# Optimization experiments

Hardware: AMD Instinct MI355X
Metric: run time of the kernel (lower is better)

## Reference

```python
import jax, jax.numpy as jnp
import numpy as np

N, IN_DIM, HID, E, NUM_TASKS, TED = 8192, 1024, 2048, 4, 8, 100
MU = 0.01
EPS = 1e-6


def setup_inputs() -> dict:
    key = jax.random.key(0)
    ks = jax.random.split(key, 8)
    s_in = 1.0 / np.sqrt(IN_DIM)
    s_h = 1.0 / np.sqrt(HID)
    return {
        "backbone_output": jax.random.normal(ks[0], (N, IN_DIM), dtype=jnp.float32),
        "task": jax.random.randint(ks[1], (N,), 0, NUM_TASKS),
        "task_embeddings": jax.random.normal(ks[2], (NUM_TASKS, TED), dtype=jnp.float32),
        "routing_matrix": jax.random.normal(ks[3], (IN_DIM + TED, E), dtype=jnp.float32) * 0.05,
        "W1": jax.random.uniform(ks[4], (E, IN_DIM, HID), jnp.float32, -s_in, s_in),
        "b1": jax.random.uniform(ks[5], (E, HID), jnp.float32, -s_in, s_in),
        "W2": jax.random.uniform(ks[6], (E, HID, HID), jnp.float32, -s_h, s_h),
        "b2": jax.random.uniform(ks[7], (E, HID), jnp.float32, -s_h, s_h),
    }


def _gram_schmidt(x):
    # x: [N, E, H] -> orthonormal basis along expert axis via sequential GS
    b0 = x[:, 0] / jnp.linalg.norm(x[:, 0], axis=-1, keepdims=True)
    basis = [b0]
    for i in range(1, x.shape[1]):
        v = x[:, i]                           # [N, H]
        B = jnp.stack(basis, axis=1)          # [N, i, H]
        coef = jnp.einsum("nh,nih->ni", v, B)
        w = v - jnp.einsum("ni,nih->nh", coef, B)
        basis.append(w / jnp.linalg.norm(w, axis=-1, keepdims=True))
    return jnp.stack(basis, axis=1)           # [N, E, H]


def reference(backbone_output, task, task_embeddings, routing_matrix, W1, b1, W2, b2):
    # router: softmax over experts on [x ; task_emb[task]] @ R
    router_in = jnp.concatenate([backbone_output, task_embeddings[task]], axis=-1)
    weights = jax.nn.softmax(router_in @ routing_matrix, axis=-1)   # [N, E]

    # per-expert 2-layer ReLU MLP, all experts at once
    h = jax.nn.relu(jnp.einsum("ni,eih->neh", backbone_output, W1) + b1[None])
    expert_outputs = jax.nn.relu(jnp.einsum("neh,ehk->nek", h, W2) + b2[None])  # [N,E,H]

    # top-1 gate: keep only max weight, zero the rest
    idx = jnp.argmax(weights, axis=-1)
    gates = jnp.where(jnp.arange(weights.shape[-1])[None, :] == idx[:, None], weights, 0.0)

    ortho = _gram_schmidt(expert_outputs)
    tower_input = jnp.einsum("ne,neh->nh", gates, ortho)

    reg_loss = -(1.0 / E) * MU * jnp.sum(jnp.log(gates + EPS), axis=-1)
    return tower_input, reg_loss
```

## Files before the change

kernel.cpp:

```cpp
#include <hip/hip_runtime.h>
#include <hip/hip_bf16.h>
#include <cstdint>

#define N_SAMP 8192
#define IN_DIM 1024
#define HID    2048
#define NE     4

typedef __attribute__((ext_vector_type(8))) __bf16 bf16x8;
typedef __attribute__((ext_vector_type(4))) float  f32x4;

#define MFMA16 __builtin_amdgcn_mfma_f32_16x16x32_bf16

__device__ __forceinline__ unsigned short f2b(float f) {
    unsigned u = __float_as_uint(f);
    u += 0x7fff + ((u >> 16) & 1);
    return (unsigned short)(u >> 16);
}
__device__ __forceinline__ float b2f(unsigned short s) {
    return __uint_as_float(((unsigned)s) << 16);
}

__device__ __forceinline__ void gll16(const void* g, void* l) {
    __builtin_amdgcn_global_load_lds(
        (const __attribute__((address_space(1))) void*)g,
        (__attribute__((address_space(3))) void*)l,
        16, 0, 0);
}

__device__ __forceinline__ int swz(int byte) {
    return byte ^ (((byte >> 7) & 7) << 4);
}

__global__ void transpose_conv(const float* __restrict__ src, unsigned short* __restrict__ dst,
                               int K, int M, size_t srcStride, size_t dstStride) {
    __shared__ float tile[64][65];
    const int e  = blockIdx.z;
    const int k0 = blockIdx.x * 64, m0 = blockIdx.y * 64;
    const int t  = threadIdx.x;
    const int tc = t & 15, tr = t >> 4;
    const float* s = src + (size_t)e * srcStride + (size_t)k0 * M + m0;
    #pragma unroll
    for (int r = tr; r < 64; r += 16) {
        float4 v = *(const float4*)&s[(size_t)r * M + tc * 4];
        tile[r][tc * 4 + 0] = v.x; tile[r][tc * 4 + 1] = v.y;
        tile[r][tc * 4 + 2] = v.z; tile[r][tc * 4 + 3] = v.w;
    }
    __syncthreads();
    unsigned short* d = dst + (size_t)e * dstStride + (size_t)m0 * K + k0;
    #pragma unroll
    for (int r = tr; r < 64; r += 16) {
        ushort4 o;
        o.x = f2b(tile[tc * 4 + 0][r]); o.y = f2b(tile[tc * 4 + 1][r]);
        o.z = f2b(tile[tc * 4 + 2][r]); o.w = f2b(tile[tc * 4 + 3][r]);
        *(ushort4*)&d[(size_t)r * K + tc * 4] = o;
    }
}

__global__ __launch_bounds__(256) void router_kernel(
    const float* __restrict__ bb, const int* __restrict__ task,
    const float* __restrict__ temb, const float* __restrict__ rm,
    unsigned short* __restrict__ Abf,
    float* __restrict__ gval, int* __restrict__ gidx,
    float* __restrict__ regout) {
    const int t = threadIdx.x, wave = t >> 6, lane = t & 63;
    const int n = blockIdx.x * 4 + wave;
    const int tk = task[n];
    float a0 = 0.f, a1 = 0.f, a2 = 0.f, a3 = 0.f;
    for (int i = lane; i < IN_DIM + 100; i += 64) {
        float x;
        if (i < IN_DIM) {
            x = bb[(size_t)n * IN_DIM + i];
            Abf[(size_t)n * IN_DIM + i] = f2b(x);
        } else {
            x = temb[tk * 100 + (i - IN_DIM)];
        }
        float4 r = *(const float4*)&rm[i * 4];
        a0 += x * r.x; a1 += x * r.y; a2 += x * r.z; a3 += x * r.w;
    }
    #pragma unroll
    for (int o = 32; o; o >>= 1) {
        a0 += __shfl_xor(a0, o); a1 += __shfl_xor(a1, o);
        a2 += __shfl_xor(a2, o); a3 += __shfl_xor(a3, o);
    }
    if (lane == 0) {
        float l[4] = {a0, a1, a2, a3};
        float mx = fmaxf(fmaxf(l[0], l[1]), fmaxf(l[2], l[3]));
        float ex[4], s = 0.f;
        #pragma unroll
        for (int j = 0; j < 4; j++) { ex[j] = expf(l[j] - mx); s += ex[j]; }
        int bi = 0; float bw = ex[0];
        #pragma unroll
        for (int j = 1; j < 4; j++) if (ex[j] > bw) { bw = ex[j]; bi = j; }
        float g = bw / s;
        gval[n] = g;
        gidx[n] = bi;
        regout[n] = -0.0025f * (logf(g + 1e-6f) + 3.0f * logf(1e-6f));
    }
}

__global__ void compact_kernel(const int* __restrict__ gidx, int* __restrict__ list,
                               int* __restrict__ pos, int* __restrict__ cnt) {
    const int e = blockIdx.x;
    const int t = threadIdx.x, lane = t & 63, wave = t >> 6;
    __shared__ int wbase[4];
    __shared__ int running;
    if (t == 0) running = 0;
    __syncthreads();
    int* le = list + (size_t)e * N_SAMP;
    int* pe = pos + (size_t)e * N_SAMP;
    for (int base = 0; base < N_SAMP; base += 256) {
        const int n = base + t;
        const bool f = gidx[n] >= e;
        unsigned long long m = __ballot(f);
        int rank = __popcll(m & ((1ULL << lane) - 1ULL));
        if (lane == 0) wbase[wave] = __popcll(m);
        __syncthreads();
        int wb = 0;
        #pragma unroll
        for (int w = 0; w < 4; w++) if (w < wave) wb += wbase[w];
        int tot = wbase[0] + wbase[1] + wbase[2] + wbase[3];
        int o = running + wb + rank;
        if (f) { le[o] = n; pe[n] = o; }
        __syncthreads();
        if (t == 0) running += tot;
        __syncthreads();
    }
    const int c = running;
    if (t == 0) cnt[e] = c;
    const int padded = (c + 255) & ~255;
    for (int i = c + t; i < padded && i < N_SAMP; i += 256) le[i] = 0;
}

template<int KT>
__device__ __forceinline__ void gemm_core(
    const unsigned short* __restrict__ A, const unsigned short* __restrict__ BT,
    const float* __restrict__ bias, unsigned short* __restrict__ C,
    int M, const int* __restrict__ rowlist, const int* __restrict__ cntp,
    int bid, char* lds_) {
    constexpr int nt = KT / 64;
    const int cnt = *cntp;
    const int mb = bid & 7, nb = bid >> 3;
    const int n0 = nb * 256;
    if (n0 >= cnt) return;
    const int m0 = mb * 256;
    const int t = threadIdx.x;
    const int w = t >> 6, lane = t & 63;
    const int wm = w >> 2, wn = w & 3;
    const int lrow = lane & 15, kg = lane >> 4;

    int rr[2], cb[2];
    #pragma unroll
    for (int q = 0; q < 2; q++) {
        int Ps = swz((t + q * 512) * 16);
        rr[q] = Ps >> 7;
        cb[q] = Ps & 127;
    }
    const char* aS[2][2];
    const char* bS[2][2];
    #pragma unroll
    for (int h = 0; h < 2; h++)
        #pragma unroll
        for (int q = 0; q < 2; q++) {
            int r = n0 + h * 128 + rr[q];
            int ga = rowlist ? rowlist[r] : r;
            aS[h][q] = (const char*)A + (size_t)ga * (KT * 2) + cb[q];
            bS[h][q] = (const char*)BT + (size_t)(m0 + h * 128 + rr[q]) * (KT * 2) + cb[q];
        }

    auto stageA = [&](int buf, int h, int kt) {
        gll16(aS[h][0] + kt * 128, lds_ + buf * 65536 + h * 16384 + w * 1024);
        gll16(aS[h][1] + kt * 128, lds_ + buf * 65536 + h * 16384 + 8192 + w * 1024);
    };
    auto stageB = [&](int buf, int h, int kt) {
        gll16(bS[h][0] + kt * 128, lds_ + buf * 65536 + 32768 + h * 16384 + w * 1024);
        gll16(bS[h][1] + kt * 128, lds_ + buf * 65536 + 32768 + h * 16384 + 8192 + w * 1024);
    };

    const int mask = (lrow & 7) << 4;
    const int c0 = (kg * 16) ^ mask;
    const int c1 = (kg * 16 + 64) ^ mask;
    const char* const pA[2] = { lds_ + wm * 16384 + lrow * 128 + c0,
                                lds_ + wm * 16384 + lrow * 128 + c1 };
    const int browB = (wn & 1) * 64 + lrow;
    const char* const pB[2] = { lds_ + 32768 + (wn >> 1) * 16384 + browB * 128 + c0,
                                lds_ + 32768 + (wn >> 1) * 16384 + browB * 128 + c1 };
    auto ldA = [&](int buf, int i, int kk) -> bf16x8 {
        return *(const bf16x8*)(pA[kk] + buf * 65536 + i * 2048);
    };
    auto ldB = [&](int buf, int j, int kk) -> bf16x8 {
        return *(const bf16x8*)(pB[kk] + buf * 65536 + j * 2048);
    };

    f32x4 acc[8][4];
    #pragma unroll
    for (int i = 0; i < 8; i++)
        #pragma unroll
        for (int j = 0; j < 4; j++) acc[i][j] = (f32x4){0.f, 0.f, 0.f, 0.f};

    stageA(0, 0, 0); stageA(0, 1, 0); stageB(0, 0, 0); stageB(0, 1, 0);
    stageA(1, 0, 1); stageA(1, 1, 1); stageB(1, 0, 1);
    asm volatile("s_waitcnt vmcnt(6)" ::: "memory");
    __builtin_amdgcn_s_barrier();

    bf16x8 af[4][2], bfr[4][2];
    auto tile = [&](int kt, int buf) {
        #pragma unroll
        for (int i = 0; i < 4; i++) { af[i][0] = ldA(buf, i, 0); af[i][1] = ldA(buf, i, 1); }
        #pragma unroll
        for (int j = 0; j < 2; j++) { bfr[j][0] = ldB(buf, j, 0); bfr[j][1] = ldB(buf, j, 1); }
        if (kt + 1 < nt) stageB(buf ^ 1, 1, kt + 1);
        __builtin_amdgcn_s_barrier();
        __builtin_amdgcn_s_setprio(1);
        #pragma unroll
        for (int i = 0; i < 4; i++)
            #pragma unroll
            for (int j = 0; j < 2; j++) {
                acc[i][j] = MFMA16(af[i][0], bfr[j][0], acc[i][j], 0, 0, 0);
                acc[i][j] = MFMA16(af[i][1], bfr[j][1], acc[i][j], 0, 0, 0);
            }
        __builtin_amdgcn_s_setprio(0);
        __builtin_amdgcn_s_barrier();
        #pragma unroll
        for (int j = 2; j < 4; j++) { bfr[j][0] = ldB(buf, j, 0); bfr[j][1] = ldB(buf, j, 1); }
        __builtin_amdgcn_s_barrier();
        __builtin_amdgcn_s_setprio(1);
        #pragma unroll
        for (int i = 0; i < 4; i++)
            #pragma unroll
            for (int j = 0; j < 2; j++) {
                acc[i][2 + j] = MFMA16(af[i][0], bfr[2 + j][0], acc[i][2 + j], 0, 0, 0);
                acc[i][2 + j] = MFMA16(af[i][1], bfr[2 + j][1], acc[i][2 + j], 0, 0, 0);
            }
        __builtin_amdgcn_s_setprio(0);
        __builtin_amdgcn_s_barrier();
        #pragma unroll
        for (int i = 0; i < 4; i++) { af[i][0] = ldA(buf, 4 + i, 0); af[i][1] = ldA(buf, 4 + i, 1); }
        if (kt + 2 < nt) stageB(buf, 0, kt + 2);
        __builtin_amdgcn_s_barrier();
        __builtin_amdgcn_s_setprio(1);
        #pragma unroll
        for (int i = 0; i < 4; i++)
            #pragma unroll
            for (int j = 0; j < 2; j++) {
                acc[4 + i][j] = MFMA16(af[i][0], bfr[j][0], acc[4 + i][j], 0, 0, 0);
                acc[4 + i][j] = MFMA16(af[i][1], bfr[j][1], acc[4 + i][j], 0, 0, 0);
            }
        __builtin_amdgcn_s_setprio(0);
        __builtin_amdgcn_s_barrier();
        if (kt + 2 < nt) { stageA(buf, 0, kt + 2); stageA(buf, 1, kt + 2); }
        __builtin_amdgcn_s_barrier();
        __builtin_amdgcn_s_setprio(1);
        #pragma unroll
        for (int i = 0; i < 4; i++)
            #pragma unroll
            for (int j = 0; j < 2; j++) {
                acc[4 + i][2 + j] = MFMA16(af[i][0], bfr[2 + j][0], acc[4 + i][2 + j], 0, 0, 0);
                acc[4 + i][2 + j] = MFMA16(af[i][1], bfr[2 + j][1], acc[4 + i][2 + j], 0, 0, 0);
            }
        __builtin_amdgcn_s_setprio(0);
        if (kt < nt - 2) asm volatile("s_waitcnt vmcnt(6)" ::: "memory");
        else             asm volatile("s_waitcnt vmcnt(0)" ::: "memory");
        __builtin_amdgcn_s_barrier();
    };
    for (int kt = 0; kt < nt; kt += 2) { tile(kt, 0); tile(kt + 1, 1); }

    float bv[4];
    #pragma unroll
    for (int j = 0; j < 4; j++)
        bv[j] = bias[m0 + wn * 64 + j * 16 + lrow];
    #pragma unroll
    for (int i = 0; i < 8; i++) {
        const int srow0 = n0 + wm * 128 + i * 16 + kg * 4;
        #pragma unroll
        for (int j = 0; j < 4; j++) {
            const int col = m0 + wn * 64 + j * 16 + lrow;
            #pragma unroll
            for (int q = 0; q < 4; q++) {
                if (srow0 + q < cnt) {
                    float x = acc[i][j][q] + bv[j];
                    C[(size_t)(srow0 + q) * M + col] = f2b(fmaxf(x, 0.f));
                }
            }
        }
    }
}

template<int KT>
__global__ __launch_bounds__(512, 2) void gemm256(
    const unsigned short* __restrict__ A, const unsigned short* __restrict__ BT,
    const float* __restrict__ bias, unsigned short* __restrict__ C,
    int M, const int* __restrict__ rowlist, const int* __restrict__ cntp) {
    extern __shared__ char lds_[];
    gemm_core<KT>(A, BT, bias, C, M, rowlist, cntp, blockIdx.x, lds_);
}

__global__ __launch_bounds__(512, 2) void gemm256_dual(
    const unsigned short* __restrict__ A2, const unsigned short* __restrict__ BT2,
    const float* __restrict__ bias2, unsigned short* __restrict__ C2,
    const int* __restrict__ cnt2,
    const unsigned short* __restrict__ A1, const unsigned short* __restrict__ BT1,
    const float* __restrict__ bias1, unsigned short* __restrict__ C1,
    const int* __restrict__ rowlist1, const int* __restrict__ cnt1) {
    extern __shared__ char lds_[];
    const int bid = blockIdx.x;
    if (bid < 256) {
        gemm_core<HID>(A2, BT2, bias2, C2, HID, nullptr, cnt2, bid, lds_);
    } else {
        gemm_core<IN_DIM>(A1, BT1, bias1, C1, HID, rowlist1, cnt1, bid - 256, lds_);
    }
}

__global__ __launch_bounds__(512, 2) void gemm256_dual_g1g1(
    const unsigned short* __restrict__ A,
    const unsigned short* __restrict__ BTa, const float* __restrict__ biasa,
    unsigned short* __restrict__ Ca, const int* __restrict__ rla, const int* __restrict__ cnta,
    const unsigned short* __restrict__ BTb, const float* __restrict__ biasb,
    unsigned short* __restrict__ Cb, const int* __restrict__ rlb, const int* __restrict__ cntb) {
    extern __shared__ char lds_[];
    const int bid = blockIdx.x;
    if (bid < 256) {
        gemm_core<IN_DIM>(A, BTa, biasa, Ca, HID, rla, cnta, bid, lds_);
    } else {
        gemm_core<IN_DIM>(A, BTb, biasb, Cb, HID, rlb, cntb, bid - 256, lds_);
    }
}

__global__ __launch_bounds__(512, 2) void gemm256_dual_g2g2(
    const unsigned short* __restrict__ Aa, const unsigned short* __restrict__ BTa,
    const float* __restrict__ biasa, unsigned short* __restrict__ Ca, const int* __restrict__ cnta,
    const unsigned short* __restrict__ Ab, const unsigned short* __restrict__ BTb,
    const float* __restrict__ biasb, unsigned short* __restrict__ Cb, const int* __restrict__ cntb) {
    extern __shared__ char lds_[];
    const int bid = blockIdx.x;
    if (bid < 256) {
        gemm_core<HID>(Aa, BTa, biasa, Ca, HID, nullptr, cnta, bid, lds_);
    } else {
        gemm_core<HID>(Ab, BTb, biasb, Cb, HID, nullptr, cntb, bid - 256, lds_);
    }
}

__global__ __launch_bounds__(256, 1) void gs_kernel(
    const unsigned short* __restrict__ eo, const float* __restrict__ gval,
    const int* __restrict__ gidx, const int* __restrict__ pos,
    float* __restrict__ dout) {
    const int t = threadIdx.x, wave = t >> 6, lane = t & 63;
    const int n = blockIdx.x * 4 + wave;
    const int idx = gidx[n];
    const float g = gval[n];

    float v[32], b0[32], b1[32], b2[32];

    auto loadv = [&](float* dst, int e) {
        const size_t row = pos[(size_t)e * N_SAMP + n];
        const unsigned short* p = eo + ((size_t)e * N_SAMP + row) * HID + lane * 8;
        #pragma unroll
        for (int c = 0; c < 4; c++) {
            uint4 u = *(const uint4*)(p + c * 512);
            const unsigned short* us = (const unsigned short*)&u;
            #pragma unroll
            for (int j = 0; j < 8; j++) dst[c * 8 + j] = b2f(us[j]);
        }
    };
    auto wdot = [&](const float* x, const float* y) -> float {
        float s = 0.f;
        #pragma unroll
        for (int k = 0; k < 32; k++) s += x[k] * y[k];
        #pragma unroll
        for (int o = 32; o; o >>= 1) s += __shfl_xor(s, o);
        return s;
    };
    auto storev = [&](const float* b) {
        float* o = dout + (size_t)n * HID + lane * 8;
        #pragma unroll
        for (int c = 0; c < 4; c++) {
            float4 x0, x1;
            x0.x = g * b[c * 8 + 0]; x0.y = g * b[c * 8 + 1];
            x0.z = g * b[c * 8 + 2]; x0.w = g * b[c * 8 + 3];
            x1.x = g * b[c * 8 + 4]; x1.y = g * b[c * 8 + 5];
            x1.z = g * b[c * 8 + 6]; x1.w = g * b[c * 8 + 7];
            *(float4*)(o + c * 512) = x0;
            *(float4*)(o + c * 512 + 4) = x1;
        }
    };

    loadv(v, 0);
    float inv = 1.f / sqrtf(wdot(v, v));
    #pragma unroll
    for (int k = 0; k < 32; k++) b0[k] = v[k] * inv;
    if (idx == 0) { storev(b0); return; }
    loadv(v, 1);
    {
        float cc0 = wdot(v, b0);
        #pragma unroll
        for (int k = 0; k < 32; k++) v[k] -= cc0 * b0[k];
        inv = 1.f / sqrtf(wdot(v, v));
        #pragma unroll
        for (int k = 0; k < 32; k++) b1[k] = v[k] * inv;
    }
    if (idx == 1) { storev(b1); return; }
    loadv(v, 2);
    {
        float cc0 = wdot(v, b0);
        float cc1 = wdot(v, b1);
        #pragma unroll
        for (int k = 0; k < 32; k++) v[k] -= cc0 * b0[k] + cc1 * b1[k];
        inv = 1.f / sqrtf(wdot(v, v));
        #pragma unroll
        for (int k = 0; k < 32; k++) b2[k] = v[k] * inv;
    }
    if (idx == 2) { storev(b2); return; }
    loadv(v, 3);
    {
        float cc0 = wdot(v, b0);
        float cc1 = wdot(v, b1);
        float cc2 = wdot(v, b2);
        #pragma unroll
        for (int k = 0; k < 32; k++) v[k] -= cc0 * b0[k] + cc1 * b1[k] + cc2 * b2[k];
        inv = 1.f / sqrtf(wdot(v, v));
        #pragma unroll
        for (int k = 0; k < 32; k++) v[k] *= inv;
    }
    storev(v);
}

extern "C" void kernel_launch(void* const* d_in, const int* in_sizes, int n_in,
                              void* d_out, int out_size, void* d_ws, size_t ws_size,
                              hipStream_t stream) {
    const float* bb   = (const float*)d_in[0];
    const int*   task = (const int*)d_in[1];
    const float* temb = (const float*)d_in[2];
    const float* rm   = (const float*)d_in[3];
    const float* W1   = (const float*)d_in[4];
    const float* b1   = (const float*)d_in[5];
    const float* W2   = (const float*)d_in[6];
    const float* b2   = (const float*)d_in[7];
    float* out = (float*)d_out;
    char* ws = (char*)d_ws;

    const size_t lds_bytes = 131072;
    const size_t W1S = (size_t)IN_DIM * HID;
    const size_t W2S = (size_t)HID * HID;
    const size_t NEED_C = 251986176;
    const size_t NEED_B = 243597376;

    if (ws_size >= NEED_B) {
        const bool planC = (ws_size >= NEED_C);
        unsigned short* obf  = (unsigned short*)(ws + 0);
        unsigned short* h0   = (unsigned short*)(ws + 33554432);
        unsigned short* h1   = (unsigned short*)(ws + 67108864);
        unsigned short* Abf  = (unsigned short*)(ws + 134217728);
        unsigned short* h2   = (unsigned short*)(ws + 150994944);
        unsigned short* h3   = (unsigned short*)(ws + 184549376);
        unsigned short* W1T  = (unsigned short*)(ws + 218103808);
        unsigned short* W2T  = (unsigned short*)(ws + 234881024);
        unsigned short* W2T23 = Abf;
        const size_t smallOfs = planC ? 251658240u : 243269632u;
        float* gv   = (float*)(ws + smallOfs);
        int*   gi   = (int*)(ws + smallOfs + 32768);
        int*   list = (int*)(ws + smallOfs + 65536);
        int*   pos  = (int*)(ws + smallOfs + 196608);
        int*   cnt  = (int*)(ws + smallOfs + 327680);

        router_kernel<<<N_SAMP / 4, 256, 0, stream>>>(bb, task, temb, rm, Abf, gv, gi,
                                                      out + (size_t)N_SAMP * HID);
        compact_kernel<<<NE, 256, 0, stream>>>(gi, list, pos, cnt);

        transpose_conv<<<dim3(IN_DIM / 64, HID / 64, NE), 256, 0, stream>>>(
            W1, W1T, IN_DIM, HID, W1S, W1S);
        if (planC) {
            transpose_conv<<<dim3(HID / 64, HID / 64, 2), 256, 0, stream>>>(
                W2, W2T, HID, HID, W2S, W2S);
        } else {
            transpose_conv<<<dim3(HID / 64, HID / 64, 1), 256, 0, stream>>>(
                W2, W2T, HID, HID, 0, 0);
        }

        gemm256_dual_g1g1<<<512, 512, lds_bytes, stream>>>(
            Abf, W1T, b1, h0, list, cnt,
            W1T + W1S, b1 + HID, h1, list + N_SAMP, cnt + 1);

        gemm256_dual<<<512, 512, lds_bytes, stream>>>(
            h0, W2T, b2, obf, cnt,
            Abf, W1T + 2 * W1S, b1 + 2 * HID, h2, list + (size_t)2 * N_SAMP, cnt + 2);

        if (!planC) {
            transpose_conv<<<dim3(HID / 64, HID / 64, 1), 256, 0, stream>>>(
                W2 + W2S, W2T, HID, HID, 0, 0);
        }
        const unsigned short* W2T1 = planC ? (W2T + W2S) : W2T;

        gemm256_dual<<<512, 512, lds_bytes, stream>>>(
            h1, W2T1, b2 + HID, obf + (size_t)1 * N_SAMP * HID, cnt + 1,
            Abf, W1T + 3 * W1S, b1 + 3 * HID, h3, list + (size_t)3 * N_SAMP, cnt + 3);

        transpose_conv<<<dim3(HID / 64, HID / 64, 2), 256, 0, stream>>>(
            W2 + 2 * W2S, W2T23, HID, HID, W2S, W2S);

        gemm256_dual_g2g2<<<512, 512, lds_bytes, stream>>>(
            h2, W2T23, b2 + 2 * HID, obf + (size_t)2 * N_SAMP * HID, cnt + 2,
            h3, W2T23 + W2S, b2 + 3 * HID, obf + (size_t)3 * N_SAMP * HID, cnt + 3);

        gs_kernel<<<N_SAMP / 4, 256, 0, stream>>>(obf, gv, gi, pos, out);
    } else {
        unsigned short* obf  = (unsigned short*)(ws + 0);
        unsigned short* Abf  = (unsigned short*)(ws + 134217728);
        unsigned short* hbfA = (unsigned short*)(ws + 150994944);
        unsigned short* W1T  = (unsigned short*)(ws + 184549376);
        unsigned short* W2T  = (unsigned short*)(ws + 188743680);
        float*          gv   = (float*)(ws + 197132288);
        int*            gi   = (int*)(ws + 197165056);
        int*            list = (int*)(ws + 197197824);
        int*            pos  = (int*)(ws + 197328896);
        int*            cnt  = (int*)(ws + 197459968);
        unsigned short* hbfB = obf + (size_t)3 * N_SAMP * HID;
        auto hbf = [&](int e) { return (e & 1) ? hbfA : hbfB; };

        router_kernel<<<N_SAMP / 4, 256, 0, stream>>>(bb, task, temb, rm, Abf, gv, gi,
                                                      out + (size_t)N_SAMP * HID);
        compact_kernel<<<NE, 256, 0, stream>>>(gi, list, pos, cnt);

        transpose_conv<<<dim3(IN_DIM / 64, HID / 64, 1), 256, 0, stream>>>(
            W1, W1T, IN_DIM, HID, 0, 0);
        gemm256<IN_DIM><<<256, 512, lds_bytes, stream>>>(
            Abf, W1T, b1, hbf(0), HID, list, cnt);

        for (int e = 0; e < 3; ++e) {
            transpose_conv<<<dim3(HID / 64, HID / 64, 1), 256, 0, stream>>>(
                W2 + (size_t)e * W2S, W2T, HID, HID, 0, 0);
            transpose_conv<<<dim3(IN_DIM / 64, HID / 64, 1), 256, 0, stream>>>(
                W1 + (size_t)(e + 1) * W1S, W1T, IN_DIM, HID, 0, 0);
            gemm256_dual<<<512, 512, lds_bytes, stream>>>(
                hbf(e), W2T, b2 + (size_t)e * HID, obf + (size_t)e * N_SAMP * HID, cnt + e,
                Abf, W1T, b1 + (size_t)(e + 1) * HID, hbf(e + 1),
                list + (size_t)(e + 1) * N_SAMP, cnt + e + 1);
        }

        transpose_conv<<<dim3(HID / 64, HID / 64, 1), 256, 0, stream>>>(
            W2 + (size_t)3 * W2S, W2T, HID, HID, 0, 0);
        gemm256<HID><<<256, 512, lds_bytes, stream>>>(
            hbf(3), W2T, b2 + (size_t)3 * HID, obf + (size_t)3 * N_SAMP * HID, HID,
            nullptr, cnt + 3);

        gs_kernel<<<N_SAMP / 4, 256, 0, stream>>>(obf, gv, gi, pos, out);
    }
}
```

Baseline: 473.6 us.

## Rebalance expert GEMM scheduling across three mixed launches with split row blocks

Adds a new workspace plan, used when the workspace is large enough, that regroups the per-expert layer-1 and layer-2 GEMMs into three mixed launches. Experts 0 and 1 have their layer-2 row blocks split between launches through a new row-block offset parameter. The aim is to fill the GPU more evenly and overlap independent expert GEMMs, cutting tail effects and launch count. The split assumes fixed block counts of 20 and 12 row-block groups per expert, and it only runs if the harness workspace exceeds the new threshold.

Measured after the change: 472.6 us. Within noise of the previous version (-0.2%).

```diff
diff --git a/kernel.cpp b/kernel.cpp
--- a/kernel.cpp
+++ b/kernel.cpp
@@ -137,10 +137,10 @@
     const unsigned short* __restrict__ A, const unsigned short* __restrict__ BT,
     const float* __restrict__ bias, unsigned short* __restrict__ C,
     int M, const int* __restrict__ rowlist, const int* __restrict__ cntp,
-    int bid, char* lds_) {
+    int bid, int nbOff, char* lds_) {
     constexpr int nt = KT / 64;
     const int cnt = *cntp;
-    const int mb = bid & 7, nb = bid >> 3;
+    const int mb = bid & 7, nb = (bid >> 3) + nbOff;
     const int n0 = nb * 256;
     if (n0 >= cnt) return;
     const int m0 = mb * 256;
@@ -292,7 +292,7 @@
     const float* __restrict__ bias, unsigned short* __restrict__ C,
     int M, const int* __restrict__ rowlist, const int* __restrict__ cntp) {
     extern __shared__ char lds_[];
-    gemm_core<KT>(A, BT, bias, C, M, rowlist, cntp, blockIdx.x, lds_);
+    gemm_core<KT>(A, BT, bias, C, M, rowlist, cntp, blockIdx.x, 0, lds_);
 }
 
 __global__ __launch_bounds__(512, 2) void gemm256_dual(
@@ -305,9 +305,9 @@
     extern __shared__ char lds_[];
     const int bid = blockIdx.x;
     if (bid < 256) {
-        gemm_core<HID>(A2, BT2, bias2, C2, HID, nullptr, cnt2, bid, lds_);
+        gemm_core<HID>(A2, BT2, bias2, C2, HID, nullptr, cnt2, bid, 0, lds_);
     } else {
-        gemm_core<IN_DIM>(A1, BT1, bias1, C1, HID, rowlist1, cnt1, bid - 256, lds_);
+        gemm_core<IN_DIM>(A1, BT1, bias1, C1, HID, rowlist1, cnt1, bid - 256, 0, lds_);
     }
 }
 
@@ -320,9 +320,9 @@
     extern __shared__ char lds_[];
     const int bid = blockIdx.x;
     if (bid < 256) {
-        gemm_core<IN_DIM>(A, BTa, biasa, Ca, HID, rla, cnta, bid, lds_);
+        gemm_core<IN_DIM>(A, BTa, biasa, Ca, HID, rla, cnta, bid, 0, lds_);
     } else {
-        gemm_core<IN_DIM>(A, BTb, biasb, Cb, HID, rlb, cntb, bid - 256, lds_);
+        gemm_core<IN_DIM>(A, BTb, biasb, Cb, HID, rlb, cntb, bid - 256, 0, lds_);
     }
 }
 
@@ -334,10 +334,48 @@
     extern __shared__ char lds_[];
     const int bid = blockIdx.x;
     if (bid < 256) {
-        gemm_core<HID>(Aa, BTa, biasa, Ca, HID, nullptr, cnta, bid, lds_);
+        gemm_core<HID>(Aa, BTa, biasa, Ca, HID, nullptr, cnta, bid, 0, lds_);
     } else {
-        gemm_core<HID>(Ab, BTb, biasb, Cb, HID, nullptr, cntb, bid - 256, lds_);
-    }
+        gemm_core<HID>(Ab, BTb, biasb, Cb, HID, nullptr, cntb, bid - 256, 0, lds_);
+    }
+}
+
+__global__ __launch_bounds__(512, 2) void gemm256_p1(
+    const unsigned short* __restrict__ h0, const unsigned short* __restrict__ W2T0,
+    const float* __restrict__ b20, unsigned short* __restrict__ obf0, const int* __restrict__ cnt0,
+    const unsigned short* __restrict__ Abf,
+    const unsigned short* __restrict__ W1T2, const float* __restrict__ b12,
+    unsigned short* __restrict__ h2, const int* __restrict__ rl2, const int* __restrict__ cnt2,
+    const unsigned short* __restrict__ W1T3, const float* __restrict__ b13,
+    unsigned short* __restrict__ h3, const int* __restrict__ rl3, const int* __restrict__ cnt3) {
+    extern __shared__ char lds_[];
+    const int bid = blockIdx.x;
+    if (bid < 160)      gemm_core<HID>(h0, W2T0, b20, obf0, HID, nullptr, cnt0, bid, 0, lds_);
+    else if (bid < 416) gemm_core<IN_DIM>(Abf, W1T2, b12, h2, HID, rl2, cnt2, bid - 160, 0, lds_);
+    else                gemm_core<IN_DIM>(Abf, W1T3, b13, h3, HID, rl3, cnt3, bid - 416, 0, lds_);
+}
+__global__ __launch_bounds__(512, 2) void gemm256_p2(
+    const unsigned short* __restrict__ h0, const unsigned short* __restrict__ W2T0,
+    const float* __restrict__ b20, unsigned short* __restrict__ obf0, const int* __restrict__ cnt0,
+    const unsigned short* __restrict__ h1, const unsigned short* __restrict__ W2T1,
+    const float* __restrict__ b21, unsigned short* __restrict__ obf1, const int* __restrict__ cnt1) {
+    extern __shared__ char lds_[];
+    const int bid = blockIdx.x;
+    if (bid < 96) gemm_core<HID>(h0, W2T0, b20, obf0, HID, nullptr, cnt0, bid, 20, lds_);
+    else          gemm_core<HID>(h1, W2T1, b21, obf1, HID, nullptr, cnt1, bid - 96, 0, lds_);
+}
+__global__ __launch_bounds__(512, 2) void gemm256_p3(
+    const unsigned short* __restrict__ h1, const unsigned short* __restrict__ W2T1,
+    const float* __restrict__ b21, unsigned short* __restrict__ obf1, const int* __restrict__ cnt1,
+    const unsigned short* __restrict__ h2, const unsigned short* __restrict__ W2T2,
+    const float* __restrict__ b22, unsigned short* __restrict__ obf2, const int* __restrict__ cnt2,
+    const unsigned short* __restrict__ h3, const unsigned short* __restrict__ W2T3,
+    const float* __restrict__ b23, unsigned short* __restrict__ obf3, const int* __restrict__ cnt3) {
+    extern __shared__ char lds_[];
+    const int bid = blockIdx.x;
+    if (bid < 96)       gemm_core<HID>(h1, W2T1, b21, obf1, HID, nullptr, cnt1, bid, 20, lds_);
+    else if (bid < 352) gemm_core<HID>(h2, W2T2, b22, obf2, HID, nullptr, cnt2, bid - 96, 0, lds_);
+    else                gemm_core<HID>(h3, W2T3, b23, obf3, HID, nullptr, cnt3, bid - 352, 0, lds_);
 }
 
 __global__ __launch_bounds__(256, 1) void gs_kernel(
@@ -441,10 +479,60 @@
     const size_t lds_bytes = 131072;
     const size_t W1S = (size_t)IN_DIM * HID;
     const size_t W2S = (size_t)HID * HID;
+    const size_t NEED_E = 277151760;
     const size_t NEED_C = 251986176;
     const size_t NEED_B = 243597376;
 
-    if (ws_size >= NEED_B) {
+    if (ws_size >= NEED_E) {
+        unsigned short* obf  = (unsigned short*)(ws + 0);
+        unsigned short* h0   = obf + (size_t)3 * N_SAMP * HID;
+        unsigned short* h1   = (unsigned short*)(ws + 134217728);
+        unsigned short* Abf  = (unsigned short*)(ws + 167772160);
+        unsigned short* h2   = (unsigned short*)(ws + 184549376);
+        unsigned short* h3   = (unsigned short*)(ws + 218103808);
+        unsigned short* W1T  = (unsigned short*)(ws + 251658240);
+        unsigned short* W2T  = (unsigned short*)(ws + 260046848);
+        unsigned short* W2T23 = Abf;
+        float* gv   = (float*)(ws + 276824064);
+        int*   gi   = (int*)(ws + 276824064 + 32768);
+        int*   list = (int*)(ws + 276824064 + 65536);
+        int*   pos  = (int*)(ws + 276824064 + 196608);
+        int*   cnt  = (int*)(ws + 276824064 + 327680);
+
+        router_kernel<<<N_SAMP / 4, 256, 0, stream>>>(bb, task, temb, rm, Abf, gv, gi,
+                                                      out + (size_t)N_SAMP * HID);
+        compact_kernel<<<NE, 256, 0, stream>>>(gi, list, pos, cnt);
+        transpose_conv<<<dim3(IN_DIM / 64, HID / 64, 2), 256, 0, stream>>>(
+            W1, W1T, IN_DIM, HID, W1S, W1S);
+        transpose_conv<<<dim3(HID / 64, HID / 64, 2), 256, 0, stream>>>(
+            W2, W2T, HID, HID, W2S, W2S);
+
+        gemm256_dual_g1g1<<<512, 512, lds_bytes, stream>>>(
+            Abf, W1T, b1, h0, list, cnt,
+            W1T + W1S, b1 + HID, h1, list + N_SAMP, cnt + 1);
+
+        transpose_conv<<<dim3(IN_DIM / 64, HID / 64, 2), 256, 0, stream>>>(
+            W1 + 2 * W1S, W1T, IN_DIM, HID, W1S, W1S);
+
+        gemm256_p1<<<672, 512, lds_bytes, stream>>>(
+            h0, W2T, b2, obf, cnt,
+            Abf, W1T, b1 + 2 * HID, h2, list + (size_t)2 * N_SAMP, cnt + 2,
+            W1T + W1S, b1 + 3 * HID, h3, list + (size_t)3 * N_SAMP, cnt + 3);
+
+        transpose_conv<<<dim3(HID / 64, HID / 64, 2), 256, 0, stream>>>(
+            W2 + 2 * W2S, W2T23, HID, HID, W2S, W2S);
+
+        gemm256_p2<<<256, 512, lds_bytes, stream>>>(
+            h0, W2T, b2, obf, cnt,
+            h1, W2T + W2S, b2 + HID, obf + (size_t)1 * N_SAMP * HID, cnt + 1);
+
+        gemm256_p3<<<608, 512, lds_bytes, stream>>>(
+            h1, W2T + W2S, b2 + HID, obf + (size_t)1 * N_SAMP * HID, cnt + 1,
+            h2, W2T23, b2 + 2 * HID, obf + (size_t)2 * N_SAMP * HID, cnt + 2,
+            h3, W2T23 + W2S, b2 + 3 * HID, obf + (size_t)3 * N_SAMP * HID, cnt + 3);
+
+        gs_kernel<<<N_SAMP / 4, 256, 0, stream>>>(obf, gv, gi, pos, out);
+    } else if (ws_size >= NEED_B) {
         const bool planC = (ws_size >= NEED_C);
         unsigned short* obf  = (unsigned short*)(ws + 0);
         unsigned short* h0   = (unsigned short*)(ws + 33554432);
```

## Reschedule expert GEMMs into three-way fused launches with new workspace layout

Applied to the files above, without the earlier changes.

The expert GEMM launches are regrouped. One kernel runs the first half of expert 0's second-layer GEMM together with the first-layer GEMMs of experts 2 and 3. A second kernel runs the remaining tiles of expert 0 plus expert 2's second layer, and a final dual launch handles experts 1 and 3. A row-block offset parameter lets one expert's GEMM be split across two launches. The workspace is repacked so hidden activations alias unused output slots and weight transposes are staged in pairs, removing the planC/planB branches. The aim is better CU occupancy per launch and more overlap of weight transposes with GEMMs, at the cost of tighter buffer aliasing that must respect the read/write ordering.

Measured after the change: 496.6 us. 4.9% more time.

```diff
diff --git a/kernel.cpp b/kernel.cpp
--- a/kernel.cpp
+++ b/kernel.cpp
@@ -137,10 +137,10 @@
     const unsigned short* __restrict__ A, const unsigned short* __restrict__ BT,
     const float* __restrict__ bias, unsigned short* __restrict__ C,
     int M, const int* __restrict__ rowlist, const int* __restrict__ cntp,
-    int bid, char* lds_) {
+    int bid, int nbOff, char* lds_) {
     constexpr int nt = KT / 64;
     const int cnt = *cntp;
-    const int mb = bid & 7, nb = bid >> 3;
+    const int mb = bid & 7, nb = (bid >> 3) + nbOff;
     const int n0 = nb * 256;
     if (n0 >= cnt) return;
     const int m0 = mb * 256;
@@ -292,7 +292,7 @@
     const float* __restrict__ bias, unsigned short* __restrict__ C,
     int M, const int* __restrict__ rowlist, const int* __restrict__ cntp) {
     extern __shared__ char lds_[];
-    gemm_core<KT>(A, BT, bias, C, M, rowlist, cntp, blockIdx.x, lds_);
+    gemm_core<KT>(A, BT, bias, C, M, rowlist, cntp, blockIdx.x, 0, lds_);
 }
 
 __global__ __launch_bounds__(512, 2) void gemm256_dual(
@@ -305,9 +305,9 @@
     extern __shared__ char lds_[];
     const int bid = blockIdx.x;
     if (bid < 256) {
-        gemm_core<HID>(A2, BT2, bias2, C2, HID, nullptr, cnt2, bid, lds_);
+        gemm_core<HID>(A2, BT2, bias2, C2, HID, nullptr, cnt2, bid, 0, lds_);
     } else {
-        gemm_core<IN_DIM>(A1, BT1, bias1, C1, HID, rowlist1, cnt1, bid - 256, lds_);
+        gemm_core<IN_DIM>(A1, BT1, bias1, C1, HID, rowlist1, cnt1, bid - 256, 0, lds_);
     }
 }
 
@@ -320,9 +320,9 @@
     extern __shared__ char lds_[];
     const int bid = blockIdx.x;
     if (bid < 256) {
-        gemm_core<IN_DIM>(A, BTa, biasa, Ca, HID, rla, cnta, bid, lds_);
+        gemm_core<IN_DIM>(A, BTa, biasa, Ca, HID, rla, cnta, bid, 0, lds_);
     } else {
-        gemm_core<IN_DIM>(A, BTb, biasb, Cb, HID, rlb, cntb, bid - 256, lds_);
+        gemm_core<IN_DIM>(A, BTb, biasb, Cb, HID, rlb, cntb, bid - 256, 0, lds_);
     }
 }
 
@@ -334,10 +334,35 @@
     extern __shared__ char lds_[];
     const int bid = blockIdx.x;
     if (bid < 256) {
-        gemm_core<HID>(Aa, BTa, biasa, Ca, HID, nullptr, cnta, bid, lds_);
+        gemm_core<HID>(Aa, BTa, biasa, Ca, HID, nullptr, cnta, bid, 0, lds_);
     } else {
-        gemm_core<HID>(Ab, BTb, biasb, Cb, HID, nullptr, cntb, bid - 256, lds_);
-    }
+        gemm_core<HID>(Ab, BTb, biasb, Cb, HID, nullptr, cntb, bid - 256, 0, lds_);
+    }
+}
+
+__global__ __launch_bounds__(512, 2) void gemm256_f1(
+    const unsigned short* __restrict__ h0, const unsigned short* __restrict__ W2T0,
+    const float* __restrict__ b20, unsigned short* __restrict__ obf0, const int* __restrict__ cnt0,
+    const unsigned short* __restrict__ Abf,
+    const unsigned short* __restrict__ W1T2, const float* __restrict__ b12,
+    unsigned short* __restrict__ h2, const int* __restrict__ rl2, const int* __restrict__ cnt2,
+    const unsigned short* __restrict__ W1T3, const float* __restrict__ b13,
+    unsigned short* __restrict__ h3, const int* __restrict__ rl3, const int* __restrict__ cnt3) {
+    extern __shared__ char lds_[];
+    const int bid = blockIdx.x;
+    if (bid < 128)      gemm_core<HID>(h0, W2T0, b20, obf0, HID, nullptr, cnt0, bid, 0, lds_);
+    else if (bid < 384) gemm_core<IN_DIM>(Abf, W1T2, b12, h2, HID, rl2, cnt2, bid - 128, 0, lds_);
+    else                gemm_core<IN_DIM>(Abf, W1T3, b13, h3, HID, rl3, cnt3, bid - 384, 0, lds_);
+}
+__global__ __launch_bounds__(512, 2) void gemm256_f2(
+    const unsigned short* __restrict__ h0, const unsigned short* __restrict__ W2T0,
+    const float* __restrict__ b20, unsigned short* __restrict__ obf0, const int* __restrict__ cnt0,
+    const unsigned short* __restrict__ h2, const unsigned short* __restrict__ W2T2,
+    const float* __restrict__ b22, unsigned short* __restrict__ obf2, const int* __restrict__ cnt2) {
+    extern __shared__ char lds_[];
+    const int bid = blockIdx.x;
+    if (bid < 128) gemm_core<HID>(h0, W2T0, b20, obf0, HID, nullptr, cnt0, bid, 16, lds_);
+    else           gemm_core<HID>(h2, W2T2, b22, obf2, HID, nullptr, cnt2, bid - 128, 0, lds_);
 }
 
 __global__ __launch_bounds__(256, 1) void gs_kernel(
@@ -441,65 +466,55 @@
     const size_t lds_bytes = 131072;
     const size_t W1S = (size_t)IN_DIM * HID;
     const size_t W2S = (size_t)HID * HID;
-    const size_t NEED_C = 251986176;
-    const size_t NEED_B = 243597376;
-
-    if (ws_size >= NEED_B) {
-        const bool planC = (ws_size >= NEED_C);
+    const size_t NEED_F = 243597376;
+
+    if (ws_size >= NEED_F) {
         unsigned short* obf  = (unsigned short*)(ws + 0);
-        unsigned short* h0   = (unsigned short*)(ws + 33554432);
-        unsigned short* h1   = (unsigned short*)(ws + 67108864);
-        unsigned short* Abf  = (unsigned short*)(ws + 134217728);
-        unsigned short* h2   = (unsigned short*)(ws + 150994944);
-        unsigned short* h3   = (unsigned short*)(ws + 184549376);
+        unsigned short* h0   = obf + (size_t)1 * N_SAMP * HID;
+        unsigned short* h2   = obf + (size_t)3 * N_SAMP * HID;
+        unsigned short* h1   = (unsigned short*)(ws + 134217728);
+        unsigned short* h3   = (unsigned short*)(ws + 167772160);
+        unsigned short* Abf  = (unsigned short*)(ws + 201326592);
         unsigned short* W1T  = (unsigned short*)(ws + 218103808);
-        unsigned short* W2T  = (unsigned short*)(ws + 234881024);
-        unsigned short* W2T23 = Abf;
-        const size_t smallOfs = planC ? 251658240u : 243269632u;
-        float* gv   = (float*)(ws + smallOfs);
-        int*   gi   = (int*)(ws + smallOfs + 32768);
-        int*   list = (int*)(ws + smallOfs + 65536);
-        int*   pos  = (int*)(ws + smallOfs + 196608);
-        int*   cnt  = (int*)(ws + smallOfs + 327680);
+        unsigned short* W2T  = (unsigned short*)(ws + 226492416);
+        unsigned short* W2T13 = Abf;
+        float* gv   = (float*)(ws + 243269632);
+        int*   gi   = (int*)(ws + 243269632 + 32768);
+        int*   list = (int*)(ws + 243269632 + 65536);
+        int*   pos  = (int*)(ws + 243269632 + 196608);
+        int*   cnt  = (int*)(ws + 243269632 + 327680);
 
         router_kernel<<<N_SAMP / 4, 256, 0, stream>>>(bb, task, temb, rm, Abf, gv, gi,
                                                       out + (size_t)N_SAMP * HID);
         compact_kernel<<<NE, 256, 0, stream>>>(gi, list, pos, cnt);
 
-        transpose_conv<<<dim3(IN_DIM / 64, HID / 64, NE), 256, 0, stream>>>(
+        transpose_conv<<<dim3(IN_DIM / 64, HID / 64, 2), 256, 0, stream>>>(
             W1, W1T, IN_DIM, HID, W1S, W1S);
-        if (planC) {
-            transpose_conv<<<dim3(HID / 64, HID / 64, 2), 256, 0, stream>>>(
-                W2, W2T, HID, HID, W2S, W2S);
-        } else {
-            transpose_conv<<<dim3(HID / 64, HID / 64, 1), 256, 0, stream>>>(
-                W2, W2T, HID, HID, 0, 0);
-        }
+        transpose_conv<<<dim3(HID / 64, HID / 64, 2), 256, 0, stream>>>(
+            W2, W2T, HID, HID, 2 * W2S, W2S);
 
         gemm256_dual_g1g1<<<512, 512, lds_bytes, stream>>>(
             Abf, W1T, b1, h0, list, cnt,
             W1T + W1S, b1 + HID, h1, list + N_SAMP, cnt + 1);
 
-        gemm256_dual<<<512, 512, lds_bytes, stream>>>(
+        transpose_conv<<<dim3(IN_DIM / 64, HID / 64, 2), 256, 0, stream>>>(
+            W1 + 2 * W1S, W1T, IN_DIM, HID, W1S, W1S);
+
+        gemm256_f1<<<640, 512, lds_bytes, stream>>>(
             h0, W2T, b2, obf, cnt,
-            Abf, W1T + 2 * W1S, b1 + 2 * HID, h2, list + (size_t)2 * N_SAMP, cnt + 2);
-
-        if (!planC) {
-            transpose_conv<<<dim3(HID / 64, HID / 64, 1), 256, 0, stream>>>(
-                W2 + W2S, W2T, HID, HID, 0, 0);
-        }
-        const unsigned short* W2T1 = planC ? (W2T + W2S) : W2T;
-
-        gemm256_dual<<<512, 512, lds_bytes, stream>>>(
-            h1, W2T1, b2 + HID, obf + (size_t)1 * N_SAMP * HID, cnt + 1,
-            Abf, W1T + 3 * W1S, b1 + 3 * HID, h3, list + (size_t)3 * N_SAMP, cnt + 3);
+            Abf, W1T, b1 + 2 * HID, h2, list + (size_t)2 * N_SAMP, cnt + 2,
+            W1T + W1S, b1 + 3 * HID, h3, list + (size_t)3 * N_SAMP, cnt + 3);
 
         transpose_conv<<<dim3(HID / 64, HID / 64, 2), 256, 0, stream>>>(
-            W2 + 2 * W2S, W2T23, HID, HID, W2S, W2S);
+            W2 + W2S, W2T13, HID, HID, 2 * W2S, W2S);
+
+        gemm256_f2<<<384, 512, lds_bytes, stream>>>(
+            h0, W2T, b2, obf, cnt,
+            h2, W2T + W2S, b2 + 2 * HID, obf + (size_t)2 * N_SAMP * HID, cnt + 2);
 
         gemm256_dual_g2g2<<<512, 512, lds_bytes, stream>>>(
-            h2, W2T23, b2 + 2 * HID, obf + (size_t)2 * N_SAMP * HID, cnt + 2,
-            h3, W2T23 + W2S, b2 + 3 * HID, obf + (size_t)3 * N_SAMP * HID, cnt + 3);
+            h1, W2T13, b2 + HID, obf + (size_t)1 * N_SAMP * HID, cnt + 1,
+            h3, W2T13 + W2S, b2 + 3 * HID, obf + (size_t)3 * N_SAMP * HID, cnt + 3);
 
         gs_kernel<<<N_SAMP / 4, 256, 0, stream>>>(obf, gv, gi, pos, out);
     } else {
```
